# Performance work log

Measured on AMD Instinct MI355X. Metric: run time of the kernel, lower is better.

Reference implementation:

```python
import jax, jax.numpy as jnp
import numpy as np

ALPHA = 0.2  # LeakyReLU negative slope
NEG_INF = -9e15


def setup_inputs() -> dict:
    key = jax.random.key(0)
    k1, k2, k3, k4 = jax.random.split(key, 4)
    B, T, N, Fin, Fout = 16, 12, 512, 64, 64
    h = jax.random.normal(k1, (B, T, N, Fin), dtype=jnp.float32)
    adj = jax.random.randint(k2, (N, N), 0, 2).astype(jnp.float32)
    W = jax.random.normal(k3, (Fin, Fout), dtype=jnp.float32) * 0.1
    a = jax.random.normal(k4, (2 * Fout, 1), dtype=jnp.float32) * 0.1
    return {"h": h, "adj": adj, "W": W, "a": a}


def reference(h, adj, W, a):
    # h: [B,T,N,Fin], adj: [N,N], W: [Fin,Fout], a: [2*Fout,1]
    Fout = W.shape[1]
    Wh = jnp.einsum('btnf,fo->btno', h, W)          # [B,T,N,Fout]
    a1 = a[:Fout, 0]                                 # [Fout]
    a2 = a[Fout:, 0]                                 # [Fout]
    Wh1 = Wh @ a1                                    # [B,T,N]
    Wh2 = Wh @ a2                                    # [B,T,N]
    e = Wh1[..., :, None] + Wh2[..., None, :]        # [B,T,N,N]
    e = jnp.where(e > 0, e, ALPHA * e)               # LeakyReLU
    att = jnp.where(adj > 0, e, NEG_INF)             # adjacency mask (broadcast)
    att = jax.nn.softmax(att, axis=-1)
    # dropout is identity in eval mode (training=False)
    h_prime = jnp.einsum('btij,btjo->btio', att, Wh)  # [B,T,N,Fout]
    return jax.nn.elu(h_prime)                        # concat=True -> ELU
```

## Files before the change

### kernel.cpp

```cpp
#include <hip/hip_runtime.h>


typedef __attribute__((ext_vector_type(8))) short short8;
typedef __attribute__((ext_vector_type(4))) float f32x4;

union U16x8 { uint4 v; short8 s; };

static __device__ __forceinline__ f32x4 mfma16(short8 a, short8 b, f32x4 c) {
    return __builtin_amdgcn_mfma_f32_16x16x32_bf16(a, b, c, 0, 0, 0);
}

static __device__ __forceinline__ void pk_hilo(float x, float y,
                                               unsigned& hw, unsigned& lw) {
    asm("v_cvt_pk_bf16_f32 %0, %1, %2" : "=v"(hw) : "v"(x), "v"(y));
    float rx = x - __uint_as_float(hw << 16);
    float ry = y - __uint_as_float(hw & 0xffff0000u);
    asm("v_cvt_pk_bf16_f32 %0, %1, %2" : "=v"(lw) : "v"(rx), "v"(ry));
}

__global__ __launch_bounds__(512)
void adj_bits_kernel(const float* __restrict__ adj, unsigned long long* __restrict__ bits)
{
    const int tid  = threadIdx.x;
    const int lane = tid & 63;
    const int w    = tid >> 6;
    const int g    = blockIdx.x * 8 + w;
    const int row  = g >> 3;
    const int k    = g & 7;
    float v = adj[row * 512 + k * 64 + lane];
    unsigned long long m = __ballot(v > 0.f);
    if (lane == 0) bits[row * 8 + k] = m;
}

__global__ __launch_bounds__(512, 2)
void gat_fused(const float* __restrict__ h, const float* __restrict__ W,
               const float* __restrict__ a,
               const unsigned long long* __restrict__ bits,
               float* __restrict__ out)
{
    __shared__ unsigned short WhH[64 * 512];
    __shared__ unsigned short WhL[64 * 512];
    __shared__ float wh1s[512];
    __shared__ float wh2s[512];
    __shared__ __align__(16) float e2p[512];
    __shared__ __align__(16) float e2n[512];

    const int tid  = threadIdx.x;
    const int lane = tid & 63;
    const int wv   = tid >> 6;
    const int col  = lane & 15;
    const int g    = lane >> 4;
    const int bt   = blockIdx.x;

    U16x8 WBh[2][4], WBl[2][4];
    #pragma unroll
    for (int kt = 0; kt < 2; ++kt) {
        #pragma unroll
        for (int ot = 0; ot < 4; ++ot) {
            const float* wp = &W[(kt * 32 + 8 * g) * 64 + ot * 16 + col];
            pk_hilo(wp[0],   wp[64],  WBh[kt][ot].v.x, WBl[kt][ot].v.x);
            pk_hilo(wp[128], wp[192], WBh[kt][ot].v.y, WBl[kt][ot].v.y);
            pk_hilo(wp[256], wp[320], WBh[kt][ot].v.z, WBl[kt][ot].v.z);
            pk_hilo(wp[384], wp[448], WBh[kt][ot].v.w, WBl[kt][ot].v.w);
        }
    }
    float a1c[4], a2c[4];
    #pragma unroll
    for (int ot = 0; ot < 4; ++ot) {
        a1c[ot] = a[ot * 16 + col];
        a2c[ot] = a[64 + ot * 16 + col];
    }

    #pragma unroll 1
    for (int mt = 0; mt < 4; ++mt) {
        const int n0w = wv * 64 + mt * 16;

        const float* hrow = &h[((size_t)bt * 512 + n0w + col) * 64];
        const float4 ha0 = *(const float4*)&hrow[8 * g];
        const float4 ha1 = *(const float4*)&hrow[8 * g + 4];
        const float4 hb0 = *(const float4*)&hrow[32 + 8 * g];
        const float4 hb1 = *(const float4*)&hrow[32 + 8 * g + 4];

        U16x8 A0h, A0l, A1h, A1l;
        pk_hilo(ha0.x, ha0.y, A0h.v.x, A0l.v.x);
        pk_hilo(ha0.z, ha0.w, A0h.v.y, A0l.v.y);
        pk_hilo(ha1.x, ha1.y, A0h.v.z, A0l.v.z);
        pk_hilo(ha1.z, ha1.w, A0h.v.w, A0l.v.w);
        pk_hilo(hb0.x, hb0.y, A1h.v.x, A1l.v.x);
        pk_hilo(hb0.z, hb0.w, A1h.v.y, A1l.v.y);
        pk_hilo(hb1.x, hb1.y, A1h.v.z, A1l.v.z);
        pk_hilo(hb1.z, hb1.w, A1h.v.w, A1l.v.w);

        f32x4 acc[4];
        #pragma unroll
        for (int ot = 0; ot < 4; ++ot) acc[ot] = (f32x4){0.f, 0.f, 0.f, 0.f};

        #pragma unroll
        for (int kt = 0; kt < 2; ++kt) {
            const short8 Ah = (kt == 0) ? A0h.s : A1h.s;
            const short8 Al = (kt == 0) ? A0l.s : A1l.s;
            #pragma unroll
            for (int ot = 0; ot < 4; ++ot) {
                acc[ot] = mfma16(Ah, WBh[kt][ot].s, acc[ot]);
                acc[ot] = mfma16(Al, WBh[kt][ot].s, acc[ot]);
                acc[ot] = mfma16(Ah, WBl[kt][ot].s, acc[ot]);
            }
        }

        #pragma unroll
        for (int r = 0; r < 4; ++r) {
            float t1 = acc[0][r] * a1c[0] + acc[1][r] * a1c[1]
                     + acc[2][r] * a1c[2] + acc[3][r] * a1c[3];
            float t2 = acc[0][r] * a2c[0] + acc[1][r] * a2c[1]
                     + acc[2][r] * a2c[2] + acc[3][r] * a2c[3];
            #pragma unroll
            for (int s = 1; s <= 8; s <<= 1) {
                t1 += __shfl_xor(t1, s);
                t2 += __shfl_xor(t2, s);
            }
            if (col == 0) {
                const int n = n0w + g * 4 + r;
                wh1s[n] = t1;
                wh2s[n] = t2;
            }
        }

        #pragma unroll
        for (int ot = 0; ot < 4; ++ot) {
            const int o = ot * 16 + col;
            unsigned h01, l01, h23, l23;
            pk_hilo(acc[ot][0], acc[ot][1], h01, l01);
            pk_hilo(acc[ot][2], acc[ot][3], h23, l23);
            const int gg = (n0w >> 3) + (g >> 1);
            const int pg = gg ^ (o & 7);
            const int el = o * 512 + pg * 8 + (g & 1) * 4;
            *(uint2*)&WhH[el] = make_uint2(h01, h23);
            *(uint2*)&WhL[el] = make_uint2(l01, l23);
        }
    }

    __syncthreads();

    {
        const float w2 = wh2s[tid];
        e2p[tid] = __expf(w2);
        e2n[tid] = __expf(0.2f * w2);
    }
    __syncthreads();

    const int rowb = wv * 64;
    float E1p[4], E1n[4], Tt[4];
    #pragma unroll
    for (int mt = 0; mt < 4; ++mt) {
        const float v = wh1s[rowb + mt * 16 + col];
        E1p[mt] = __expf(v);
        E1n[mt] = __expf(0.2f * v);
        Tt[mt]  = __expf(-v);
    }

    short8 ones;
    #pragma unroll
    for (int r = 0; r < 8; ++r) ones[r] = (short)0x3F80;

    f32x4 acc[4][4];
    f32x4 sacc[4];
    #pragma unroll
    for (int mt = 0; mt < 4; ++mt) {
        sacc[mt] = (f32x4){0.f, 0.f, 0.f, 0.f};
        #pragma unroll
        for (int ot = 0; ot < 4; ++ot) acc[mt][ot] = (f32x4){0.f, 0.f, 0.f, 0.f};
    }

    const unsigned* b32 = (const unsigned*)bits;

    #pragma unroll 1
    for (int kk = 0; kk < 16; ++kk) {
        const int k0 = kk * 32;

        U16x8 Bh[4], Bl[4];
        #pragma unroll
        for (int ot = 0; ot < 4; ++ot) {
            const int o  = ot * 16 + col;
            const int el = o * 512 + (((kk * 4 + g) ^ (o & 7)) << 3);
            Bh[ot].v = *(const uint4*)&WhH[el];
            Bl[ot].v = *(const uint4*)&WhL[el];
        }

        const float4 epa = *(const float4*)&e2p[k0 + 8 * g];
        const float4 epb = *(const float4*)&e2p[k0 + 8 * g + 4];
        const float4 ena = *(const float4*)&e2n[k0 + 8 * g];
        const float4 enb = *(const float4*)&e2n[k0 + 8 * g + 4];
        const float ep8[8] = {epa.x, epa.y, epa.z, epa.w, epb.x, epb.y, epb.z, epb.w};
        const float en8[8] = {ena.x, ena.y, ena.z, ena.w, enb.x, enb.y, enb.z, enb.w};

        U16x8 Ah[4], Al[4];
        #pragma unroll
        for (int mt = 0; mt < 4; ++mt) {
            const int row = rowb + mt * 16 + col;
            const unsigned w  = b32[(size_t)row * 16 + kk];
            const unsigned mb = (w >> (8 * g)) & 0xffu;
            float pv[8];
            #pragma unroll
            for (int r = 0; r < 8; ++r) {
                const bool c = ep8[r] > Tt[mt];
                float p = (c ? E1p[mt] : E1n[mt]) * (c ? ep8[r] : en8[r]);
                pv[r] = ((mb >> r) & 1u) ? p : 0.f;
            }
            pk_hilo(pv[0], pv[1], Ah[mt].v.x, Al[mt].v.x);
            pk_hilo(pv[2], pv[3], Ah[mt].v.y, Al[mt].v.y);
            pk_hilo(pv[4], pv[5], Ah[mt].v.z, Al[mt].v.z);
            pk_hilo(pv[6], pv[7], Ah[mt].v.w, Al[mt].v.w);
        }

        #pragma unroll
        for (int mt = 0; mt < 4; ++mt) {
            sacc[mt] = mfma16(Ah[mt].s, ones, sacc[mt]);
            sacc[mt] = mfma16(Al[mt].s, ones, sacc[mt]);
        }
        #pragma unroll
        for (int mt = 0; mt < 4; ++mt) {
            #pragma unroll
            for (int ot = 0; ot < 4; ++ot) {
                acc[mt][ot] = mfma16(Ah[mt].s, Bh[ot].s, acc[mt][ot]);
                acc[mt][ot] = mfma16(Al[mt].s, Bh[ot].s, acc[mt][ot]);
                acc[mt][ot] = mfma16(Ah[mt].s, Bl[ot].s, acc[mt][ot]);
            }
        }
    }

    const size_t ob = (size_t)bt * 32768;
    #pragma unroll
    for (int mt = 0; mt < 4; ++mt) {
        float inv[4];
        #pragma unroll
        for (int r = 0; r < 4; ++r) inv[r] = 1.f / sacc[mt][r];
        #pragma unroll
        for (int ot = 0; ot < 4; ++ot) {
            #pragma unroll
            for (int r = 0; r < 4; ++r) {
                float v = acc[mt][ot][r] * inv[r];
                v = (v > 0.f) ? v : __expf(v) - 1.f;
                const int rowi = rowb + mt * 16 + g * 4 + r;
                out[ob + (size_t)rowi * 64 + ot * 16 + col] = v;
            }
        }
    }
}

extern "C" void kernel_launch(void* const* d_in, const int* in_sizes, int n_in,
                              void* d_out, int out_size, void* d_ws, size_t ws_size,
                              hipStream_t stream)
{
    const float* h   = (const float*)d_in[0];
    const float* adj = (const float*)d_in[1];
    const float* W   = (const float*)d_in[2];
    const float* a   = (const float*)d_in[3];
    float* out = (float*)d_out;

    unsigned long long* bits = (unsigned long long*)d_ws;

    adj_bits_kernel<<<512, 512, 0, stream>>>(adj, bits);
    gat_fused<<<192, 512, 0, stream>>>(h, W, a, bits, out);
}
```

Before: 117.1 us.

## Double block to 1024 threads with 32 rows per wave and vectorized mask loads

Launches the fused GAT kernel with 1024 threads per block, so each of 16 waves handles 32 output rows instead of 64. The goal is more resident waves per CU to hide LDS and MFMA latency. Adjacency bitmask words are now fetched four at a time as a uint4, and the Wh B-fragments are loaded from LDS inside the output-tile loop instead of being preloaded. The cost is twice the LDS reads of Wh per block, since each wave reuses a B fragment over fewer rows. The stricter launch bounds of (1024, 4) may also squeeze the register budget and cause spills.

```diff
diff --git a/kernel.cpp b/kernel.cpp
--- a/kernel.cpp
+++ b/kernel.cpp
@@ -32,7 +32,7 @@
     if (lane == 0) bits[row * 8 + k] = m;
 }
 
-__global__ __launch_bounds__(512, 2)
+__global__ __launch_bounds__(1024, 4)
 void gat_fused(const float* __restrict__ h, const float* __restrict__ W,
                const float* __restrict__ a,
                const unsigned long long* __restrict__ bits,
@@ -72,8 +72,8 @@
     }
 
     #pragma unroll 1
-    for (int mt = 0; mt < 4; ++mt) {
-        const int n0w = wv * 64 + mt * 16;
+    for (int mt = 0; mt < 2; ++mt) {
+        const int n0w = wv * 32 + mt * 16;
 
         const float* hrow = &h[((size_t)bt * 512 + n0w + col) * 64];
         const float4 ha0 = *(const float4*)&hrow[8 * g];
@@ -141,17 +141,17 @@
 
     __syncthreads();
 
-    {
+    if (tid < 512) {
         const float w2 = wh2s[tid];
         e2p[tid] = __expf(w2);
         e2n[tid] = __expf(0.2f * w2);
     }
     __syncthreads();
 
-    const int rowb = wv * 64;
-    float E1p[4], E1n[4], Tt[4];
-    #pragma unroll
-    for (int mt = 0; mt < 4; ++mt) {
+    const int rowb = wv * 32;
+    float E1p[2], E1n[2], Tt[2];
+    #pragma unroll
+    for (int mt = 0; mt < 2; ++mt) {
         const float v = wh1s[rowb + mt * 16 + col];
         E1p[mt] = __expf(v);
         E1n[mt] = __expf(0.2f * v);
@@ -162,75 +162,87 @@
     #pragma unroll
     for (int r = 0; r < 8; ++r) ones[r] = (short)0x3F80;
 
-    f32x4 acc[4][4];
-    f32x4 sacc[4];
-    #pragma unroll
-    for (int mt = 0; mt < 4; ++mt) {
+    f32x4 acc[2][4];
+    f32x4 sacc[2];
+    #pragma unroll
+    for (int mt = 0; mt < 2; ++mt) {
         sacc[mt] = (f32x4){0.f, 0.f, 0.f, 0.f};
         #pragma unroll
         for (int ot = 0; ot < 4; ++ot) acc[mt][ot] = (f32x4){0.f, 0.f, 0.f, 0.f};
     }
 
     const unsigned* b32 = (const unsigned*)bits;
+    const int row0 = rowb + col;
+    const int row1 = row0 + 16;
 
     #pragma unroll 1
-    for (int kk = 0; kk < 16; ++kk) {
-        const int k0 = kk * 32;
-
-        U16x8 Bh[4], Bl[4];
-        #pragma unroll
-        for (int ot = 0; ot < 4; ++ot) {
-            const int o  = ot * 16 + col;
-            const int el = o * 512 + (((kk * 4 + g) ^ (o & 7)) << 3);
-            Bh[ot].v = *(const uint4*)&WhH[el];
-            Bl[ot].v = *(const uint4*)&WhL[el];
-        }
-
-        const float4 epa = *(const float4*)&e2p[k0 + 8 * g];
-        const float4 epb = *(const float4*)&e2p[k0 + 8 * g + 4];
-        const float4 ena = *(const float4*)&e2n[k0 + 8 * g];
-        const float4 enb = *(const float4*)&e2n[k0 + 8 * g + 4];
-        const float ep8[8] = {epa.x, epa.y, epa.z, epa.w, epb.x, epb.y, epb.z, epb.w};
-        const float en8[8] = {ena.x, ena.y, ena.z, ena.w, enb.x, enb.y, enb.z, enb.w};
-
-        U16x8 Ah[4], Al[4];
-        #pragma unroll
-        for (int mt = 0; mt < 4; ++mt) {
-            const int row = rowb + mt * 16 + col;
-            const unsigned w  = b32[(size_t)row * 16 + kk];
-            const unsigned mb = (w >> (8 * g)) & 0xffu;
-            float pv[8];
-            #pragma unroll
-            for (int r = 0; r < 8; ++r) {
-                const bool c = ep8[r] > Tt[mt];
-                float p = (c ? E1p[mt] : E1n[mt]) * (c ? ep8[r] : en8[r]);
-                pv[r] = ((mb >> r) & 1u) ? p : 0.f;
-            }
-            pk_hilo(pv[0], pv[1], Ah[mt].v.x, Al[mt].v.x);
-            pk_hilo(pv[2], pv[3], Ah[mt].v.y, Al[mt].v.y);
-            pk_hilo(pv[4], pv[5], Ah[mt].v.z, Al[mt].v.z);
-            pk_hilo(pv[6], pv[7], Ah[mt].v.w, Al[mt].v.w);
-        }
-
-        #pragma unroll
-        for (int mt = 0; mt < 4; ++mt) {
-            sacc[mt] = mfma16(Ah[mt].s, ones, sacc[mt]);
-            sacc[mt] = mfma16(Al[mt].s, ones, sacc[mt]);
-        }
-        #pragma unroll
-        for (int mt = 0; mt < 4; ++mt) {
+    for (int ko = 0; ko < 4; ++ko) {
+        const uint4 wA4 = *(const uint4*)&b32[(size_t)row0 * 16 + ko * 4];
+        const uint4 wB4 = *(const uint4*)&b32[(size_t)row1 * 16 + ko * 4];
+        const unsigned wa[4] = {wA4.x, wA4.y, wA4.z, wA4.w};
+        const unsigned wb[4] = {wB4.x, wB4.y, wB4.z, wB4.w};
+
+        #pragma unroll
+        for (int ki = 0; ki < 4; ++ki) {
+            const int kk = ko * 4 + ki;
+            const int k0 = kk * 32;
+
+            const float4 epa = *(const float4*)&e2p[k0 + 8 * g];
+            const float4 epb = *(const float4*)&e2p[k0 + 8 * g + 4];
+            const float4 ena = *(const float4*)&e2n[k0 + 8 * g];
+            const float4 enb = *(const float4*)&e2n[k0 + 8 * g + 4];
+            const float ep8[8] = {epa.x, epa.y, epa.z, epa.w, epb.x, epb.y, epb.z, epb.w};
+            const float en8[8] = {ena.x, ena.y, ena.z, ena.w, enb.x, enb.y, enb.z, enb.w};
+            const unsigned mb0 = (wa[ki] >> (8 * g)) & 0xffu;
+            const unsigned mb1 = (wb[ki] >> (8 * g)) & 0xffu;
+
+            U16x8 Ah[2], Al[2];
+            {
+                float pv0[8], pv1[8];
+                #pragma unroll
+                for (int r = 0; r < 8; ++r) {
+                    const bool c0 = ep8[r] > Tt[0];
+                    float p0 = (c0 ? E1p[0] : E1n[0]) * (c0 ? ep8[r] : en8[r]);
+                    pv0[r] = ((mb0 >> r) & 1u) ? p0 : 0.f;
+                    const bool c1 = ep8[r] > Tt[1];
+                    float p1 = (c1 ? E1p[1] : E1n[1]) * (c1 ? ep8[r] : en8[r]);
+                    pv1[r] = ((mb1 >> r) & 1u) ? p1 : 0.f;
+                }
+                pk_hilo(pv0[0], pv0[1], Ah[0].v.x, Al[0].v.x);
+                pk_hilo(pv0[2], pv0[3], Ah[0].v.y, Al[0].v.y);
+                pk_hilo(pv0[4], pv0[5], Ah[0].v.z, Al[0].v.z);
+                pk_hilo(pv0[6], pv0[7], Ah[0].v.w, Al[0].v.w);
+                pk_hilo(pv1[0], pv1[1], Ah[1].v.x, Al[1].v.x);
+                pk_hilo(pv1[2], pv1[3], Ah[1].v.y, Al[1].v.y);
+                pk_hilo(pv1[4], pv1[5], Ah[1].v.z, Al[1].v.z);
+                pk_hilo(pv1[6], pv1[7], Ah[1].v.w, Al[1].v.w);
+            }
+
+            sacc[0] = mfma16(Ah[0].s, ones, sacc[0]);
+            sacc[0] = mfma16(Al[0].s, ones, sacc[0]);
+            sacc[1] = mfma16(Ah[1].s, ones, sacc[1]);
+            sacc[1] = mfma16(Al[1].s, ones, sacc[1]);
+
             #pragma unroll
             for (int ot = 0; ot < 4; ++ot) {
-                acc[mt][ot] = mfma16(Ah[mt].s, Bh[ot].s, acc[mt][ot]);
-                acc[mt][ot] = mfma16(Al[mt].s, Bh[ot].s, acc[mt][ot]);
-                acc[mt][ot] = mfma16(Ah[mt].s, Bl[ot].s, acc[mt][ot]);
+                const int o  = ot * 16 + col;
+                const int el = o * 512 + (((kk * 4 + g) ^ (o & 7)) << 3);
+                U16x8 Bh, Bl;
+                Bh.v = *(const uint4*)&WhH[el];
+                Bl.v = *(const uint4*)&WhL[el];
+                acc[0][ot] = mfma16(Ah[0].s, Bh.s, acc[0][ot]);
+                acc[0][ot] = mfma16(Al[0].s, Bh.s, acc[0][ot]);
+                acc[0][ot] = mfma16(Ah[0].s, Bl.s, acc[0][ot]);
+                acc[1][ot] = mfma16(Ah[1].s, Bh.s, acc[1][ot]);
+                acc[1][ot] = mfma16(Al[1].s, Bh.s, acc[1][ot]);
+                acc[1][ot] = mfma16(Ah[1].s, Bl.s, acc[1][ot]);
             }
         }
     }
 
     const size_t ob = (size_t)bt * 32768;
     #pragma unroll
-    for (int mt = 0; mt < 4; ++mt) {
+    for (int mt = 0; mt < 2; ++mt) {
         float inv[4];
         #pragma unroll
         for (int r = 0; r < 4; ++r) inv[r] = 1.f / sacc[mt][r];
@@ -260,5 +272,5 @@
     unsigned long long* bits = (unsigned long long*)d_ws;
 
     adj_bits_kernel<<<512, 512, 0, stream>>>(adj, bits);
-    gat_fused<<<192, 512, 0, stream>>>(h, W, a, bits, out);
-}
+    gat_fused<<<192, 1024, 0, stream>>>(h, W, a, bits, out);
+}
```

Result: faster. 112.1 us (-4.3%).

## Split attention K dimension across two wave groups with 1024-thread blocks

Applied to the files above, without the earlier changes.

Doubles the block to 1024 threads so each row group of 64 rows is handled by two waves, each covering half of the neighbor (K) range. Partial accumulators and row sums are then reduced through shared memory in two staged passes that reuse the Wh buffer. The aim is more waves per CU to hide latency, since there are only 192 blocks. Bitmask loads are also vectorized to uint4 per 4 k-steps, and B fragments are loaded per output tile. The cost is extra synchronisation and a shared-memory reduction, plus tighter register limits at 1024 threads that may cause spills.

```diff
diff --git a/kernel.cpp b/kernel.cpp
--- a/kernel.cpp
+++ b/kernel.cpp
@@ -32,18 +32,20 @@
     if (lane == 0) bits[row * 8 + k] = m;
 }
 
-__global__ __launch_bounds__(512, 2)
+__global__ __launch_bounds__(1024)
 void gat_fused(const float* __restrict__ h, const float* __restrict__ W,
                const float* __restrict__ a,
                const unsigned long long* __restrict__ bits,
                float* __restrict__ out)
 {
-    __shared__ unsigned short WhH[64 * 512];
-    __shared__ unsigned short WhL[64 * 512];
+    __shared__ unsigned short WhB[2 * 64 * 512];
     __shared__ float wh1s[512];
     __shared__ float wh2s[512];
     __shared__ __align__(16) float e2p[512];
     __shared__ __align__(16) float e2n[512];
+
+    unsigned short* uH = WhB;
+    unsigned short* uL = WhB + 64 * 512;
 
     const int tid  = threadIdx.x;
     const int lane = tid & 63;
@@ -72,8 +74,8 @@
     }
 
     #pragma unroll 1
-    for (int mt = 0; mt < 4; ++mt) {
-        const int n0w = wv * 64 + mt * 16;
+    for (int mt = 0; mt < 2; ++mt) {
+        const int n0w = wv * 32 + mt * 16;
 
         const float* hrow = &h[((size_t)bt * 512 + n0w + col) * 64];
         const float4 ha0 = *(const float4*)&hrow[8 * g];
@@ -134,21 +136,24 @@
             const int gg = (n0w >> 3) + (g >> 1);
             const int pg = gg ^ (o & 7);
             const int el = o * 512 + pg * 8 + (g & 1) * 4;
-            *(uint2*)&WhH[el] = make_uint2(h01, h23);
-            *(uint2*)&WhL[el] = make_uint2(l01, l23);
-        }
-    }
-
-    __syncthreads();
-
-    {
+            *(uint2*)&uH[el] = make_uint2(h01, h23);
+            *(uint2*)&uL[el] = make_uint2(l01, l23);
+        }
+    }
+
+    __syncthreads();
+
+    if (tid < 512) {
         const float w2 = wh2s[tid];
         e2p[tid] = __expf(w2);
         e2n[tid] = __expf(0.2f * w2);
     }
     __syncthreads();
 
-    const int rowb = wv * 64;
+    const int rg   = wv & 7;
+    const int kh   = wv >> 3;
+    const int rowb = rg * 64;
+
     float E1p[4], E1n[4], Tt[4];
     #pragma unroll
     for (int mt = 0; mt < 4; ++mt) {
@@ -172,76 +177,149 @@
     }
 
     const unsigned* b32 = (const unsigned*)bits;
+    const int kw0 = kh * 8;
 
     #pragma unroll 1
-    for (int kk = 0; kk < 16; ++kk) {
-        const int k0 = kk * 32;
-
-        U16x8 Bh[4], Bl[4];
-        #pragma unroll
-        for (int ot = 0; ot < 4; ++ot) {
-            const int o  = ot * 16 + col;
-            const int el = o * 512 + (((kk * 4 + g) ^ (o & 7)) << 3);
-            Bh[ot].v = *(const uint4*)&WhH[el];
-            Bl[ot].v = *(const uint4*)&WhL[el];
-        }
-
-        const float4 epa = *(const float4*)&e2p[k0 + 8 * g];
-        const float4 epb = *(const float4*)&e2p[k0 + 8 * g + 4];
-        const float4 ena = *(const float4*)&e2n[k0 + 8 * g];
-        const float4 enb = *(const float4*)&e2n[k0 + 8 * g + 4];
-        const float ep8[8] = {epa.x, epa.y, epa.z, epa.w, epb.x, epb.y, epb.z, epb.w};
-        const float en8[8] = {ena.x, ena.y, ena.z, ena.w, enb.x, enb.y, enb.z, enb.w};
-
-        U16x8 Ah[4], Al[4];
-        #pragma unroll
-        for (int mt = 0; mt < 4; ++mt) {
-            const int row = rowb + mt * 16 + col;
-            const unsigned w  = b32[(size_t)row * 16 + kk];
-            const unsigned mb = (w >> (8 * g)) & 0xffu;
-            float pv[8];
-            #pragma unroll
-            for (int r = 0; r < 8; ++r) {
-                const bool c = ep8[r] > Tt[mt];
-                float p = (c ? E1p[mt] : E1n[mt]) * (c ? ep8[r] : en8[r]);
-                pv[r] = ((mb >> r) & 1u) ? p : 0.f;
-            }
-            pk_hilo(pv[0], pv[1], Ah[mt].v.x, Al[mt].v.x);
-            pk_hilo(pv[2], pv[3], Ah[mt].v.y, Al[mt].v.y);
-            pk_hilo(pv[4], pv[5], Ah[mt].v.z, Al[mt].v.z);
-            pk_hilo(pv[6], pv[7], Ah[mt].v.w, Al[mt].v.w);
-        }
-
-        #pragma unroll
-        for (int mt = 0; mt < 4; ++mt) {
-            sacc[mt] = mfma16(Ah[mt].s, ones, sacc[mt]);
-            sacc[mt] = mfma16(Al[mt].s, ones, sacc[mt]);
-        }
-        #pragma unroll
-        for (int mt = 0; mt < 4; ++mt) {
+    for (int ko = 0; ko < 2; ++ko) {
+        uint4 w40 = *(const uint4*)&b32[(size_t)(rowb + col)      * 16 + kw0 + ko * 4];
+        uint4 w41 = *(const uint4*)&b32[(size_t)(rowb + 16 + col) * 16 + kw0 + ko * 4];
+        uint4 w42 = *(const uint4*)&b32[(size_t)(rowb + 32 + col) * 16 + kw0 + ko * 4];
+        uint4 w43 = *(const uint4*)&b32[(size_t)(rowb + 48 + col) * 16 + kw0 + ko * 4];
+        const unsigned wm[4][4] = {
+            {w40.x, w40.y, w40.z, w40.w},
+            {w41.x, w41.y, w41.z, w41.w},
+            {w42.x, w42.y, w42.z, w42.w},
+            {w43.x, w43.y, w43.z, w43.w}};
+
+        #pragma unroll
+        for (int ki = 0; ki < 4; ++ki) {
+            const int k0 = kh * 256 + (ko * 4 + ki) * 32;
+
+            const float4 epa = *(const float4*)&e2p[k0 + 8 * g];
+            const float4 epb = *(const float4*)&e2p[k0 + 8 * g + 4];
+            const float4 ena = *(const float4*)&e2n[k0 + 8 * g];
+            const float4 enb = *(const float4*)&e2n[k0 + 8 * g + 4];
+            const float ep8[8] = {epa.x, epa.y, epa.z, epa.w, epb.x, epb.y, epb.z, epb.w};
+            const float en8[8] = {ena.x, ena.y, ena.z, ena.w, enb.x, enb.y, enb.z, enb.w};
+
+            U16x8 Ah[4], Al[4];
+            #pragma unroll
+            for (int mt = 0; mt < 4; ++mt) {
+                const unsigned mb = (wm[mt][ki] >> (8 * g)) & 0xffu;
+                float pv[8];
+                #pragma unroll
+                for (int r = 0; r < 8; ++r) {
+                    const bool c = ep8[r] > Tt[mt];
+                    float p = (c ? E1p[mt] : E1n[mt]) * (c ? ep8[r] : en8[r]);
+                    pv[r] = ((mb >> r) & 1u) ? p : 0.f;
+                }
+                pk_hilo(pv[0], pv[1], Ah[mt].v.x, Al[mt].v.x);
+                pk_hilo(pv[2], pv[3], Ah[mt].v.y, Al[mt].v.y);
+                pk_hilo(pv[4], pv[5], Ah[mt].v.z, Al[mt].v.z);
+                pk_hilo(pv[6], pv[7], Ah[mt].v.w, Al[mt].v.w);
+            }
+
+            #pragma unroll
+            for (int mt = 0; mt < 4; ++mt) {
+                sacc[mt] = mfma16(Ah[mt].s, ones, sacc[mt]);
+                sacc[mt] = mfma16(Al[mt].s, ones, sacc[mt]);
+            }
+
             #pragma unroll
             for (int ot = 0; ot < 4; ++ot) {
-                acc[mt][ot] = mfma16(Ah[mt].s, Bh[ot].s, acc[mt][ot]);
-                acc[mt][ot] = mfma16(Al[mt].s, Bh[ot].s, acc[mt][ot]);
-                acc[mt][ot] = mfma16(Ah[mt].s, Bl[ot].s, acc[mt][ot]);
-            }
-        }
-    }
-
-    const size_t ob = (size_t)bt * 32768;
-    #pragma unroll
-    for (int mt = 0; mt < 4; ++mt) {
-        float inv[4];
-        #pragma unroll
-        for (int r = 0; r < 4; ++r) inv[r] = 1.f / sacc[mt][r];
-        #pragma unroll
-        for (int ot = 0; ot < 4; ++ot) {
-            #pragma unroll
-            for (int r = 0; r < 4; ++r) {
-                float v = acc[mt][ot][r] * inv[r];
-                v = (v > 0.f) ? v : __expf(v) - 1.f;
-                const int rowi = rowb + mt * 16 + g * 4 + r;
-                out[ob + (size_t)rowi * 64 + ot * 16 + col] = v;
+                const int o  = ot * 16 + col;
+                const int el = o * 512 + ((((k0 >> 3) + g) ^ (o & 7)) << 3);
+                U16x8 Bh, Bl;
+                Bh.v = *(const uint4*)&uH[el];
+                Bl.v = *(const uint4*)&uL[el];
+                #pragma unroll
+                for (int mt = 0; mt < 4; ++mt) {
+                    acc[mt][ot] = mfma16(Ah[mt].s, Bh.s, acc[mt][ot]);
+                    acc[mt][ot] = mfma16(Al[mt].s, Bh.s, acc[mt][ot]);
+                    acc[mt][ot] = mfma16(Ah[mt].s, Bl.s, acc[mt][ot]);
+                }
+            }
+        }
+    }
+
+    float* fs = (float*)WhB;
+    __syncthreads();
+    if (kh == 1 && rg < 4) {
+        const int base = rg * 80;
+        #pragma unroll
+        for (int mt = 0; mt < 4; ++mt) {
+            #pragma unroll
+            for (int ot = 0; ot < 4; ++ot)
+                #pragma unroll
+                for (int r = 0; r < 4; ++r)
+                    fs[(base + (mt * 4 + ot) * 4 + r) * 64 + lane] = acc[mt][ot][r];
+            #pragma unroll
+            for (int r = 0; r < 4; ++r)
+                fs[(base + 64 + mt * 4 + r) * 64 + lane] = sacc[mt][r];
+        }
+    }
+    __syncthreads();
+    if (kh == 0 && rg < 4) {
+        const int base = rg * 80;
+        #pragma unroll
+        for (int mt = 0; mt < 4; ++mt) {
+            #pragma unroll
+            for (int ot = 0; ot < 4; ++ot)
+                #pragma unroll
+                for (int r = 0; r < 4; ++r)
+                    acc[mt][ot][r] += fs[(base + (mt * 4 + ot) * 4 + r) * 64 + lane];
+            #pragma unroll
+            for (int r = 0; r < 4; ++r)
+                sacc[mt][r] += fs[(base + 64 + mt * 4 + r) * 64 + lane];
+        }
+    }
+    __syncthreads();
+    if (kh == 1 && rg >= 4) {
+        const int base = (rg - 4) * 80;
+        #pragma unroll
+        for (int mt = 0; mt < 4; ++mt) {
+            #pragma unroll
+            for (int ot = 0; ot < 4; ++ot)
+                #pragma unroll
+                for (int r = 0; r < 4; ++r)
+                    fs[(base + (mt * 4 + ot) * 4 + r) * 64 + lane] = acc[mt][ot][r];
+            #pragma unroll
+            for (int r = 0; r < 4; ++r)
+                fs[(base + 64 + mt * 4 + r) * 64 + lane] = sacc[mt][r];
+        }
+    }
+    __syncthreads();
+    if (kh == 0 && rg >= 4) {
+        const int base = (rg - 4) * 80;
+        #pragma unroll
+        for (int mt = 0; mt < 4; ++mt) {
+            #pragma unroll
+            for (int ot = 0; ot < 4; ++ot)
+                #pragma unroll
+                for (int r = 0; r < 4; ++r)
+                    acc[mt][ot][r] += fs[(base + (mt * 4 + ot) * 4 + r) * 64 + lane];
+            #pragma unroll
+            for (int r = 0; r < 4; ++r)
+                sacc[mt][r] += fs[(base + 64 + mt * 4 + r) * 64 + lane];
+        }
+    }
+
+    if (kh == 0) {
+        const size_t ob = (size_t)bt * 32768;
+        #pragma unroll
+        for (int mt = 0; mt < 4; ++mt) {
+            float inv[4];
+            #pragma unroll
+            for (int r = 0; r < 4; ++r) inv[r] = 1.f / sacc[mt][r];
+            #pragma unroll
+            for (int ot = 0; ot < 4; ++ot) {
+                #pragma unroll
+                for (int r = 0; r < 4; ++r) {
+                    float v = acc[mt][ot][r] * inv[r];
+                    v = (v > 0.f) ? v : __expf(v) - 1.f;
+                    const int rowi = rowb + mt * 16 + g * 4 + r;
+                    out[ob + (size_t)rowi * 64 + ot * 16 + col] = v;
+                }
             }
         }
     }
@@ -260,5 +338,5 @@
     unsigned long long* bits = (unsigned long long*)d_ws;
 
     adj_bits_kernel<<<512, 512, 0, stream>>>(adj, bits);
-    gat_fused<<<192, 512, 0, stream>>>(h, W, a, bits, out);
-}
+    gat_fused<<<192, 1024, 0, stream>>>(h, W, a, bits, out);
+}
```

New measurement: 180.9 us. 54.5% more time.
